# Kernel optimization log

Measured on AMD Instinct MI355X. Metric: run time of the kernel, lower is better.

Reference implementation:

```python
import jax, jax.numpy as jnp
import numpy as np

N_NODES = 20000
N_EDGES = 320000
HIDDEN = 256
N_GRAPHS = 64
IN_DIM = 3
OUT_DIM = 2


def _glorot(key, shape):
    fan_in, fan_out = shape
    lim = jnp.sqrt(6.0 / (fan_in + fan_out))
    return jax.random.uniform(key, shape, jnp.float32, -lim, lim)


def setup_inputs() -> dict:
    key = jax.random.key(0)
    ks = jax.random.split(key, 16)
    inp = {
        "x": jax.random.normal(ks[0], (N_NODES, IN_DIM), jnp.float32),
        "edge_index": jax.random.randint(ks[1], (2, N_EDGES), 0, N_NODES, jnp.int64),
        "batch": jnp.sort(jax.random.randint(ks[2], (N_NODES,), 0, N_GRAPHS, jnp.int64)),
        "W1": _glorot(ks[3], (IN_DIM, HIDDEN)), "b1": jnp.zeros((HIDDEN,), jnp.float32),
        "W2": _glorot(ks[4], (HIDDEN, HIDDEN)), "b2": jnp.zeros((HIDDEN,), jnp.float32),
        "W3": _glorot(ks[5], (HIDDEN, HIDDEN)), "b3": jnp.zeros((HIDDEN,), jnp.float32),
        "W4": _glorot(ks[6], (HIDDEN, HIDDEN)), "b4": jnp.zeros((HIDDEN,), jnp.float32),
        "W5": _glorot(ks[7], (HIDDEN, HIDDEN)), "b5": jnp.zeros((HIDDEN,), jnp.float32),
        "Wlin": _glorot(ks[8], (HIDDEN, OUT_DIM)), "blin": jnp.zeros((OUT_DIM,), jnp.float32),
    }
    return inp


def _gcn_norm(edge_index, n_nodes):
    # PyG GCNConv default: add self-loops, symmetric degree normalization.
    loops = jnp.arange(n_nodes, dtype=edge_index.dtype)
    src = jnp.concatenate([edge_index[0], loops])
    dst = jnp.concatenate([edge_index[1], loops])
    deg = jax.ops.segment_sum(jnp.ones_like(dst, jnp.float32), dst, num_segments=n_nodes)
    dinv = jnp.where(deg > 0, jax.lax.rsqrt(deg), 0.0)
    norm = dinv[src] * dinv[dst]  # [E + N]
    return src, dst, norm


def _gcn_layer(x, W, b, src, dst, norm, n_nodes):
    h = x @ W                                   # [N, H]
    msg = h[src] * norm[:, None]                # [E+N, H] gather + scale
    agg = jax.ops.segment_sum(msg, dst, num_segments=n_nodes)  # scatter-add
    return agg + b


def reference(x, edge_index, batch, W1, b1, W2, b2, W3, b3, W4, b4, W5, b5, Wlin, blin):
    n = x.shape[0]
    src, dst, norm = _gcn_norm(edge_index, n)
    h = jax.nn.relu(_gcn_layer(x, W1, b1, src, dst, norm, n))
    h = jax.nn.relu(_gcn_layer(h, W2, b2, src, dst, norm, n))
    h = jax.nn.relu(_gcn_layer(h, W3, b3, src, dst, norm, n))
    h = jax.nn.relu(_gcn_layer(h, W4, b4, src, dst, norm, n))
    h = jax.nn.relu(_gcn_layer(h, W5, b5, src, dst, norm, n))
    pooled = jax.ops.segment_sum(h, batch, num_segments=N_GRAPHS)  # global_add_pool
    return pooled @ Wlin + blin
```

## Files before the change

kernel.cpp:

```cpp
#include <hip/hip_runtime.h>

#define N_NODES 20000
#define N_PAD 20096
#define N_EDGES 320000
#define HIDDEN 256
#define N_GRAPHS 64
#define OUT_DIM 2

#define QPANEL_BYTES 65536
#define QTABLE_BYTES 32768
#define GEMM_GRID 628

typedef __attribute__((ext_vector_type(8))) short short8v;
typedef __attribute__((ext_vector_type(4))) float f32x4;
typedef __attribute__((ext_vector_type(4))) unsigned short us4;

__global__ void k_zero(int* __restrict__ degi, float* __restrict__ pooled) {
    int i = blockIdx.x * 256 + threadIdx.x;
    if (i < N_NODES) degi[i] = 0;
    if (i < N_GRAPHS * HIDDEN) pooled[i] = 0.f;
}

__global__ void k_degree(const int* __restrict__ dst, int* __restrict__ degi) {
    int e = blockIdx.x * blockDim.x + threadIdx.x;
    if (e < N_EDGES) atomicAdd(&degi[dst[e]], 1);
}

__global__ void k_scan(const int* __restrict__ degi, int* __restrict__ rowptr,
                       int* __restrict__ rowstart, float* __restrict__ dinv) {
    __shared__ int sums[1024];
    int t = threadIdx.x;
    int base = t * 20;
    int ld[20];
    int local = 0;
    if (t < 1000) {
#pragma unroll
        for (int i = 0; i < 20; ++i) {
            ld[i] = degi[base + i];
            local += ld[i];
            dinv[base + i] = rsqrtf((float)ld[i] + 1.0f);
        }
    }
    sums[t] = local;
    __syncthreads();
    for (int off = 1; off < 1024; off <<= 1) {
        int v = (t >= off) ? sums[t - off] : 0;
        __syncthreads();
        sums[t] += v;
        __syncthreads();
    }
    if (t < 1000) {
        int run = (t == 0) ? 0 : sums[t - 1];
#pragma unroll
        for (int i = 0; i < 20; ++i) {
            rowptr[base + i] = run;
            rowstart[base + i] = run;
            run += ld[i];
        }
    }
    if (t == 1023) rowptr[N_NODES] = sums[1023];
}

__global__ void k_fill(const int* __restrict__ src, const int* __restrict__ dst,
                       const float* __restrict__ dinv, int* __restrict__ rowstart,
                       int2* __restrict__ csr) {
    int e = blockIdx.x * blockDim.x + threadIdx.x;
    if (e >= N_EDGES) return;
    int s = src[e], d = dst[e];
    int pos = atomicAdd(&rowstart[d], 1);
    csr[pos] = make_int2(s, __float_as_int(dinv[s] * dinv[d]));
}

__global__ void k_wprep4(const float* __restrict__ W2, const float* __restrict__ W3,
                         const float* __restrict__ W4, const float* __restrict__ W5,
                         char* __restrict__ wt) {
    int lid = blockIdx.x >> 8;
    int idx = (blockIdx.x & 255) * 256 + threadIdx.x;
    const float* W = lid == 0 ? W2 : lid == 1 ? W3 : lid == 2 ? W4 : W5;
    int k = idx & 255, n = idx >> 8;
    float a = W[k * 256 + n];
    unsigned u = __float_as_uint(a);
    ushort hi = (ushort)(u >> 16);
    float hif = __uint_as_float(u & 0xffff0000u);
    ushort lo = (ushort)(__float_as_uint(a - hif) >> 16);
    int q = n >> 6, colQ = n & 63, slab = k >> 3, e = k & 7;
    size_t base = ((size_t)lid * 4 + q) * QPANEL_BYTES;
    size_t soff = (size_t)slab * 1024 + ((colQ * 16 + slab * 32) & 1023) + e * 2;
    *(ushort*)(wt + base + soff) = hi;
    *(ushort*)(wt + base + QTABLE_BYTES + soff) = lo;
}

__global__ void k_aggx(const float* __restrict__ x, const float* __restrict__ dinv,
                       const int* __restrict__ rowptr, const int2* __restrict__ csr,
                       float* __restrict__ z) {
    int t = blockIdx.x * blockDim.x + threadIdx.x;
    int i = t >> 2, c = t & 3;
    if (i >= N_NODES || c >= 3) return;
    float di = dinv[i];
    float a = di * di * x[i * 3 + c], bacc = 0.f;
    int k = rowptr[i], end = rowptr[i + 1];
    for (; k + 1 < end; k += 2) {
        int2 e0 = csr[k], e1 = csr[k + 1];
        a = fmaf(x[(size_t)e0.x * 3 + c], __int_as_float(e0.y), a);
        bacc = fmaf(x[(size_t)e1.x * 3 + c], __int_as_float(e1.y), bacc);
    }
    if (k < end) {
        int2 e0 = csr[k];
        a = fmaf(x[(size_t)e0.x * 3 + c], __int_as_float(e0.y), a);
    }
    z[i * 3 + c] = a + bacc;
}

__global__ void k_h1(const float* __restrict__ z, const float* __restrict__ W1,
                     const float* __restrict__ b1,
                     ushort* __restrict__ out_hi, ushort* __restrict__ out_lo) {
    int i = blockIdx.x;
    int j = threadIdx.x;
    float z0 = z[i * 3], z1 = z[i * 3 + 1], z2 = z[i * 3 + 2];
    float v = fmaf(z0, W1[j], fmaf(z1, W1[256 + j], fmaf(z2, W1[512 + j], b1[j])));
    v = fmaxf(v, 0.0f);
    unsigned u = __float_as_uint(v);
    ushort hi = (ushort)(u >> 16);
    float hif = __uint_as_float(u & 0xffff0000u);
    ushort lo = (ushort)(__float_as_uint(v - hif) >> 16);
    out_hi[(size_t)i * HIDDEN + j] = hi;
    out_lo[(size_t)i * HIDDEN + j] = lo;
}

__global__ void k_csr_agg(const float* __restrict__ h, const float* __restrict__ dinv,
                          const int* __restrict__ rowptr, const int2* __restrict__ csr,
                          const float* __restrict__ b,
                          ushort* __restrict__ out_hi, ushort* __restrict__ out_lo) {
    int bid = blockIdx.x;
    int slice = bid & 7;
    int node = (bid >> 3) * 32 + (threadIdx.x >> 3);
    int cl = threadIdx.x & 7;
    int scol = slice * 32 + cl * 4;
    int beg = rowptr[node], end = rowptr[node + 1];
    float4 A0 = {0.f, 0.f, 0.f, 0.f}, A1 = {0.f, 0.f, 0.f, 0.f};
    int k = beg;
    for (; k + 1 < end; k += 2) {
        int2 e0 = csr[k], e1 = csr[k + 1];
        float w0 = __int_as_float(e0.y), w1 = __int_as_float(e1.y);
        float4 v0 = *reinterpret_cast<const float4*>(h + (size_t)e0.x * HIDDEN + scol);
        float4 v1 = *reinterpret_cast<const float4*>(h + (size_t)e1.x * HIDDEN + scol);
        A0.x = fmaf(v0.x, w0, A0.x);  A1.x = fmaf(v1.x, w1, A1.x);
        A0.y = fmaf(v0.y, w0, A0.y);  A1.y = fmaf(v1.y, w1, A1.y);
        A0.z = fmaf(v0.z, w0, A0.z);  A1.z = fmaf(v1.z, w1, A1.z);
        A0.w = fmaf(v0.w, w0, A0.w);  A1.w = fmaf(v1.w, w1, A1.w);
    }
    if (k < end) {
        int2 e0 = csr[k];
        float w0 = __int_as_float(e0.y);
        float4 v0 = *reinterpret_cast<const float4*>(h + (size_t)e0.x * HIDDEN + scol);
        A0.x = fmaf(v0.x, w0, A0.x);
        A0.y = fmaf(v0.y, w0, A0.y);
        A0.z = fmaf(v0.z, w0, A0.z);
        A0.w = fmaf(v0.w, w0, A0.w);
    }
    float di = dinv[node];
    float ws = di * di;
    float4 bv = *reinterpret_cast<const float4*>(b + scol);
    float4 hv = *reinterpret_cast<const float4*>(h + (size_t)node * HIDDEN + scol);
    float rv[4];
    rv[0] = fmaxf(fmaf(hv.x, ws, bv.x + A0.x + A1.x), 0.f);
    rv[1] = fmaxf(fmaf(hv.y, ws, bv.y + A0.y + A1.y), 0.f);
    rv[2] = fmaxf(fmaf(hv.z, ws, bv.z + A0.z + A1.z), 0.f);
    rv[3] = fmaxf(fmaf(hv.w, ws, bv.w + A0.w + A1.w), 0.f);
    us4 hvv, lvv;
#pragma unroll
    for (int j = 0; j < 4; ++j) {
        unsigned u = __float_as_uint(rv[j]);
        hvv[j] = (ushort)(u >> 16);
        float hif = __uint_as_float(u & 0xffff0000u);
        lvv[j] = (ushort)(__float_as_uint(rv[j] - hif) >> 16);
    }
    *reinterpret_cast<us4*>(out_hi + (size_t)node * HIDDEN + scol) = hvv;
    *reinterpret_cast<us4*>(out_lo + (size_t)node * HIDDEN + scol) = lvv;
}

__global__ __launch_bounds__(512) void k_gemm_mfma(const ushort* __restrict__ a_hi,
                                                   const ushort* __restrict__ a_lo,
                                                   const char* __restrict__ wpanels,
                                                   float* __restrict__ out) {
    __shared__ char smem[QPANEL_BYTES];
    int d = blockIdx.x;
    int xcd = d & 7, idx = d >> 3;
    const int q0 = GEMM_GRID / 8, r = GEMM_GRID % 8;
    int base = xcd * q0 + (xcd < r ? xcd : r);
    int logical = base + idx;
    int mtile = logical >> 2, q = logical & 3;

    const char* gsrc = wpanels + (size_t)q * QPANEL_BYTES;
    int tid = threadIdx.x;
#pragma unroll
    for (int it = 0; it < 8; ++it) {
        int o = it * 8192 + tid * 16;
        *reinterpret_cast<float4*>(smem + o) = *reinterpret_cast<const float4*>(gsrc + o);
    }
    __syncthreads();

    int w = tid >> 6, l = tid & 63;
    int lr = l & 15, kg = l >> 4;
    int wm = w >> 1, wn = w & 1;
    int row0 = mtile * 128 + wm * 32;
    int colQ0 = wn * 32;

    const ushort* aph = a_hi + (size_t)(row0 + lr) * HIDDEN + kg * 8;
    const ushort* apl = a_lo + (size_t)(row0 + lr) * HIDDEN + kg * 8;

    short8v ah0 = *reinterpret_cast<const short8v*>(aph);
    short8v ah1 = *reinterpret_cast<const short8v*>(aph + 16 * HIDDEN);
    short8v al0 = *reinterpret_cast<const short8v*>(apl);
    short8v al1 = *reinterpret_cast<const short8v*>(apl + 16 * HIDDEN);

    f32x4 acc[2][2] = {};
#pragma unroll
    for (int t = 0; t < 8; ++t) {
        short8v cah0 = ah0, cah1 = ah1, cal0 = al0, cal1 = al1;
        if (t < 7) {
            int kb = (t + 1) * 32;
            ah0 = *reinterpret_cast<const short8v*>(aph + kb);
            ah1 = *reinterpret_cast<const short8v*>(aph + 16 * HIDDEN + kb);
            al0 = *reinterpret_cast<const short8v*>(apl + kb);
            al1 = *reinterpret_cast<const short8v*>(apl + 16 * HIDDEN + kb);
        }
        int slab = t * 4 + kg;
        int sbase = slab * 1024;
        int rot = slab * 32;
        int off0 = sbase + (((colQ0 + lr) * 16 + rot) & 1023);
        int off1 = sbase + (((colQ0 + 16 + lr) * 16 + rot) & 1023);
        short8v bh0 = *reinterpret_cast<const short8v*>(smem + off0);
        short8v bh1 = *reinterpret_cast<const short8v*>(smem + off1);
        short8v bl0 = *reinterpret_cast<const short8v*>(smem + QTABLE_BYTES + off0);
        short8v bl1 = *reinterpret_cast<const short8v*>(smem + QTABLE_BYTES + off1);
        acc[0][0] = __builtin_amdgcn_mfma_f32_16x16x32_bf16(cah0, bh0, acc[0][0], 0, 0, 0);
        acc[1][0] = __builtin_amdgcn_mfma_f32_16x16x32_bf16(cah1, bh0, acc[1][0], 0, 0, 0);
        acc[0][1] = __builtin_amdgcn_mfma_f32_16x16x32_bf16(cah0, bh1, acc[0][1], 0, 0, 0);
        acc[1][1] = __builtin_amdgcn_mfma_f32_16x16x32_bf16(cah1, bh1, acc[1][1], 0, 0, 0);
        acc[0][0] = __builtin_amdgcn_mfma_f32_16x16x32_bf16(cal0, bh0, acc[0][0], 0, 0, 0);
        acc[1][0] = __builtin_amdgcn_mfma_f32_16x16x32_bf16(cal1, bh0, acc[1][0], 0, 0, 0);
        acc[0][1] = __builtin_amdgcn_mfma_f32_16x16x32_bf16(cal0, bh1, acc[0][1], 0, 0, 0);
        acc[1][1] = __builtin_amdgcn_mfma_f32_16x16x32_bf16(cal1, bh1, acc[1][1], 0, 0, 0);
        acc[0][0] = __builtin_amdgcn_mfma_f32_16x16x32_bf16(cah0, bl0, acc[0][0], 0, 0, 0);
        acc[1][0] = __builtin_amdgcn_mfma_f32_16x16x32_bf16(cah1, bl0, acc[1][0], 0, 0, 0);
        acc[0][1] = __builtin_amdgcn_mfma_f32_16x16x32_bf16(cah0, bl1, acc[0][1], 0, 0, 0);
        acc[1][1] = __builtin_amdgcn_mfma_f32_16x16x32_bf16(cah1, bl1, acc[1][1], 0, 0, 0);
    }
    int gcol = q * 64 + colQ0 + lr;
#pragma unroll
    for (int rf = 0; rf < 2; ++rf) {
        float* o0 = out + (size_t)(row0 + rf * 16 + kg * 4) * HIDDEN + gcol;
#pragma unroll
        for (int rr = 0; rr < 4; ++rr)
#pragma unroll
            for (int cf = 0; cf < 2; ++cf)
                o0[(size_t)rr * HIDDEN + cf * 16] = acc[rf][cf][rr];
    }
}

__global__ void k_pool(const ushort* __restrict__ hi, const ushort* __restrict__ lo,
                       const int* __restrict__ batch, float* __restrict__ pooled) {
    int base = blockIdx.x * 32;
    int j = threadIdx.x;
    float acc = 0.0f;
    int cur = batch[base];
    for (int r = 0; r < 32; ++r) {
        int i = base + r;
        int bg = batch[i];
        if (bg != cur) {
            atomicAdd(&pooled[cur * HIDDEN + j], acc);
            acc = 0.0f;
            cur = bg;
        }
        size_t off = (size_t)i * HIDDEN + j;
        float v = __uint_as_float((unsigned)hi[off] << 16) +
                  __uint_as_float((unsigned)lo[off] << 16);
        acc += v;
    }
    atomicAdd(&pooled[cur * HIDDEN + j], acc);
}

__global__ void k_final(const float* __restrict__ pooled, const float* __restrict__ Wlin,
                        const float* __restrict__ blin, float* __restrict__ out) {
    int t = threadIdx.x;
    int g = t >> 1, o = t & 1;
    float s = blin[o];
    for (int k = 0; k < HIDDEN; ++k) s += pooled[g * HIDDEN + k] * Wlin[k * OUT_DIM + o];
    out[g * OUT_DIM + o] = s;
}

extern "C" void kernel_launch(void* const* d_in, const int* in_sizes, int n_in,
                              void* d_out, int out_size, void* d_ws, size_t ws_size,
                              hipStream_t stream) {
    const float* x     = (const float*)d_in[0];
    const int*   esrc  = (const int*)d_in[1];
    const int*   edst  = esrc + N_EDGES;
    const int*   batch = (const int*)d_in[2];
    const float* W1 = (const float*)d_in[3];
    const float* b1 = (const float*)d_in[4];
    const float* W2 = (const float*)d_in[5];
    const float* b2 = (const float*)d_in[6];
    const float* W3 = (const float*)d_in[7];
    const float* b3 = (const float*)d_in[8];
    const float* W4 = (const float*)d_in[9];
    const float* b4 = (const float*)d_in[10];
    const float* W5 = (const float*)d_in[11];
    const float* b5 = (const float*)d_in[12];
    const float* Wlin = (const float*)d_in[13];
    const float* blin = (const float*)d_in[14];
    float* out = (float*)d_out;

    char* ws = (char*)d_ws;
    size_t off = 0;
    auto alloc = [&](size_t bytes) { size_t o = off; off += (bytes + 255) & ~size_t(255); return (void*)(ws + o); };

    int*    degi     = (int*)alloc(N_NODES * 4);
    float*  dinv     = (float*)alloc(N_NODES * 4);
    int*    rowptr   = (int*)alloc((N_NODES + 1) * 4);
    int*    rowstart = (int*)alloc(N_NODES * 4);
    int2*   csr      = (int2*)alloc((size_t)N_EDGES * 8);
    float*  hA       = (float*)alloc((size_t)N_PAD * HIDDEN * 4);
    ushort* hb_hi    = (ushort*)alloc((size_t)N_PAD * HIDDEN * 2);
    ushort* hb_lo    = (ushort*)alloc((size_t)N_PAD * HIDDEN * 2);
    float*  pooled   = (float*)alloc(N_GRAPHS * HIDDEN * 4);
    char*   wt       = (char*)alloc((size_t)4 * 4 * QPANEL_BYTES);
    float*  z        = (float*)alloc((size_t)N_NODES * 3 * 4);

    k_zero<<<(N_NODES + 255) / 256, 256, 0, stream>>>(degi, pooled);
    k_degree<<<(N_EDGES + 255) / 256, 256, 0, stream>>>(edst, degi);
    k_scan<<<1, 1024, 0, stream>>>(degi, rowptr, rowstart, dinv);
    k_fill<<<(N_EDGES + 255) / 256, 256, 0, stream>>>(esrc, edst, dinv, rowstart, csr);
    k_wprep4<<<1024, 256, 0, stream>>>(W2, W3, W4, W5, wt);

    const float* bs[5] = {b1, b2, b3, b4, b5};

    k_aggx<<<(N_NODES * 4 + 255) / 256, 256, 0, stream>>>(x, dinv, rowptr, csr, z);
    k_h1<<<N_NODES, HIDDEN, 0, stream>>>(z, W1, b1, hb_hi, hb_lo);

    for (int l = 1; l < 5; ++l) {
        k_gemm_mfma<<<GEMM_GRID, 512, 0, stream>>>(
            hb_hi, hb_lo, wt + (size_t)(l - 1) * 4 * QPANEL_BYTES, hA);
        k_csr_agg<<<(N_NODES / 32) * 8, 256, 0, stream>>>(hA, dinv, rowptr, csr, bs[l], hb_hi, hb_lo);
    }

    k_pool<<<N_NODES / 32, HIDDEN, 0, stream>>>(hb_hi, hb_lo, batch, pooled);
    k_final<<<1, 128, 0, stream>>>(pooled, Wlin, blin, out);
}
```

Measured before the change: 363.3 us.

## Sort nodes by degree for aggregation, unroll gather by four, fuse prep kernels

Builds a degree-bucketed permutation of nodes, using a histogram in the scan kernel and a counting-sort scatter in the fill kernel. Aggregation blocks then process nodes of similar degree together, which cuts wavefront divergence from uneven edge counts. The gather loop is unrolled to four independent accumulators so more loads are in flight. The degree count is merged with weight prep, and the node permutation with the CSR fill, to save launches. The cost is an extra indirection through perm and scattered output writes, since rows are no longer written in node order.

```diff
diff --git a/kernel.cpp b/kernel.cpp
--- a/kernel.cpp
+++ b/kernel.cpp
@@ -21,61 +21,19 @@
     if (i < N_GRAPHS * HIDDEN) pooled[i] = 0.f;
 }
 
-__global__ void k_degree(const int* __restrict__ dst, int* __restrict__ degi) {
-    int e = blockIdx.x * blockDim.x + threadIdx.x;
-    if (e < N_EDGES) atomicAdd(&degi[dst[e]], 1);
-}
-
-__global__ void k_scan(const int* __restrict__ degi, int* __restrict__ rowptr,
-                       int* __restrict__ rowstart, float* __restrict__ dinv) {
-    __shared__ int sums[1024];
-    int t = threadIdx.x;
-    int base = t * 20;
-    int ld[20];
-    int local = 0;
-    if (t < 1000) {
-#pragma unroll
-        for (int i = 0; i < 20; ++i) {
-            ld[i] = degi[base + i];
-            local += ld[i];
-            dinv[base + i] = rsqrtf((float)ld[i] + 1.0f);
-        }
-    }
-    sums[t] = local;
-    __syncthreads();
-    for (int off = 1; off < 1024; off <<= 1) {
-        int v = (t >= off) ? sums[t - off] : 0;
-        __syncthreads();
-        sums[t] += v;
-        __syncthreads();
-    }
-    if (t < 1000) {
-        int run = (t == 0) ? 0 : sums[t - 1];
-#pragma unroll
-        for (int i = 0; i < 20; ++i) {
-            rowptr[base + i] = run;
-            rowstart[base + i] = run;
-            run += ld[i];
-        }
-    }
-    if (t == 1023) rowptr[N_NODES] = sums[1023];
-}
-
-__global__ void k_fill(const int* __restrict__ src, const int* __restrict__ dst,
-                       const float* __restrict__ dinv, int* __restrict__ rowstart,
-                       int2* __restrict__ csr) {
-    int e = blockIdx.x * blockDim.x + threadIdx.x;
-    if (e >= N_EDGES) return;
-    int s = src[e], d = dst[e];
-    int pos = atomicAdd(&rowstart[d], 1);
-    csr[pos] = make_int2(s, __float_as_int(dinv[s] * dinv[d]));
-}
-
-__global__ void k_wprep4(const float* __restrict__ W2, const float* __restrict__ W3,
-                         const float* __restrict__ W4, const float* __restrict__ W5,
-                         char* __restrict__ wt) {
-    int lid = blockIdx.x >> 8;
-    int idx = (blockIdx.x & 255) * 256 + threadIdx.x;
+__global__ void k_degree_wprep(const int* __restrict__ dst, int* __restrict__ degi,
+                               const float* __restrict__ W2, const float* __restrict__ W3,
+                               const float* __restrict__ W4, const float* __restrict__ W5,
+                               char* __restrict__ wt) {
+    int bid = blockIdx.x;
+    if (bid < 1250) {
+        int e = bid * 256 + threadIdx.x;
+        if (e < N_EDGES) atomicAdd(&degi[dst[e]], 1);
+        return;
+    }
+    int wb = bid - 1250;
+    int lid = wb >> 8;
+    int idx = (wb & 255) * 256 + threadIdx.x;
     const float* W = lid == 0 ? W2 : lid == 1 ? W3 : lid == 2 ? W4 : W5;
     int k = idx & 255, n = idx >> 8;
     float a = W[k * 256 + n];
@@ -88,6 +46,72 @@
     size_t soff = (size_t)slab * 1024 + ((colQ * 16 + slab * 32) & 1023) + e * 2;
     *(ushort*)(wt + base + soff) = hi;
     *(ushort*)(wt + base + QTABLE_BYTES + soff) = lo;
+}
+
+__global__ void k_scan(const int* __restrict__ degi, int* __restrict__ rowptr,
+                       int* __restrict__ rowstart, float* __restrict__ dinv,
+                       int* __restrict__ binstart) {
+    __shared__ int sums[1024];
+    __shared__ int bins[256];
+    int t = threadIdx.x;
+    if (t < 256) bins[t] = 0;
+    __syncthreads();
+    int base = t * 20;
+    int ld[20];
+    int local = 0;
+    if (t < 1000) {
+#pragma unroll
+        for (int i = 0; i < 20; ++i) {
+            ld[i] = degi[base + i];
+            local += ld[i];
+            dinv[base + i] = rsqrtf((float)ld[i] + 1.0f);
+            atomicAdd(&bins[ld[i] < 255 ? ld[i] : 255], 1);
+        }
+    }
+    sums[t] = local;
+    __syncthreads();
+    for (int off = 1; off < 1024; off <<= 1) {
+        int v = (t >= off) ? sums[t - off] : 0;
+        __syncthreads();
+        sums[t] += v;
+        __syncthreads();
+    }
+    if (t < 1000) {
+        int run = (t == 0) ? 0 : sums[t - 1];
+#pragma unroll
+        for (int i = 0; i < 20; ++i) {
+            rowptr[base + i] = run;
+            rowstart[base + i] = run;
+            run += ld[i];
+        }
+    }
+    if (t == 1023) rowptr[N_NODES] = sums[1023];
+    __syncthreads();
+    if (t == 0) {
+        int run = 0;
+        for (int i = 0; i < 256; ++i) { binstart[i] = run; run += bins[i]; }
+    }
+}
+
+__global__ void k_fill(const int* __restrict__ src, const int* __restrict__ dst,
+                       const float* __restrict__ dinv, int* __restrict__ rowstart,
+                       int2* __restrict__ csr, const int* __restrict__ degi,
+                       int* __restrict__ binstart, int* __restrict__ perm) {
+    int bid = blockIdx.x;
+    if (bid < 1250) {
+        int e = bid * 256 + threadIdx.x;
+        if (e >= N_EDGES) return;
+        int s = src[e], d = dst[e];
+        int pos = atomicAdd(&rowstart[d], 1);
+        csr[pos] = make_int2(s, __float_as_int(dinv[s] * dinv[d]));
+        return;
+    }
+    int i = (bid - 1250) * 256 + threadIdx.x;
+    if (i < N_NODES) {
+        int d = degi[i]; d = d < 255 ? d : 255;
+        int pos = atomicAdd(&binstart[d], 1);
+        perm[pos] = i;
+    }
 }
 
 __global__ void k_aggx(const float* __restrict__ x, const float* __restrict__ dinv,
@@ -129,17 +153,35 @@
 
 __global__ void k_csr_agg(const float* __restrict__ h, const float* __restrict__ dinv,
                           const int* __restrict__ rowptr, const int2* __restrict__ csr,
-                          const float* __restrict__ b,
+                          const float* __restrict__ b, const int* __restrict__ perm,
                           ushort* __restrict__ out_hi, ushort* __restrict__ out_lo) {
     int bid = blockIdx.x;
     int slice = bid & 7;
-    int node = (bid >> 3) * 32 + (threadIdx.x >> 3);
+    int nidx = (bid >> 3) * 32 + (threadIdx.x >> 3);
+    int node = perm[nidx];
     int cl = threadIdx.x & 7;
     int scol = slice * 32 + cl * 4;
     int beg = rowptr[node], end = rowptr[node + 1];
-    float4 A0 = {0.f, 0.f, 0.f, 0.f}, A1 = {0.f, 0.f, 0.f, 0.f};
+    float4 A0 = {0,0,0,0}, A1 = {0,0,0,0}, A2 = {0,0,0,0}, A3 = {0,0,0,0};
     int k = beg;
-    for (; k + 1 < end; k += 2) {
+    for (; k + 3 < end; k += 4) {
+        int2 e0 = csr[k], e1 = csr[k + 1], e2 = csr[k + 2], e3 = csr[k + 3];
+        float w0 = __int_as_float(e0.y), w1 = __int_as_float(e1.y);
+        float w2 = __int_as_float(e2.y), w3 = __int_as_float(e3.y);
+        float4 v0 = *reinterpret_cast<const float4*>(h + (size_t)e0.x * HIDDEN + scol);
+        float4 v1 = *reinterpret_cast<const float4*>(h + (size_t)e1.x * HIDDEN + scol);
+        float4 v2 = *reinterpret_cast<const float4*>(h + (size_t)e2.x * HIDDEN + scol);
+        float4 v3 = *reinterpret_cast<const float4*>(h + (size_t)e3.x * HIDDEN + scol);
+        A0.x = fmaf(v0.x, w0, A0.x);  A1.x = fmaf(v1.x, w1, A1.x);
+        A0.y = fmaf(v0.y, w0, A0.y);  A1.y = fmaf(v1.y, w1, A1.y);
+        A0.z = fmaf(v0.z, w0, A0.z);  A1.z = fmaf(v1.z, w1, A1.z);
+        A0.w = fmaf(v0.w, w0, A0.w);  A1.w = fmaf(v1.w, w1, A1.w);
+        A2.x = fmaf(v2.x, w2, A2.x);  A3.x = fmaf(v3.x, w3, A3.x);
+        A2.y = fmaf(v2.y, w2, A2.y);  A3.y = fmaf(v3.y, w3, A3.y);
+        A2.z = fmaf(v2.z, w2, A2.z);  A3.z = fmaf(v3.z, w3, A3.z);
+        A2.w = fmaf(v2.w, w2, A2.w);  A3.w = fmaf(v3.w, w3, A3.w);
+    }
+    if (k + 1 < end) {
         int2 e0 = csr[k], e1 = csr[k + 1];
         float w0 = __int_as_float(e0.y), w1 = __int_as_float(e1.y);
         float4 v0 = *reinterpret_cast<const float4*>(h + (size_t)e0.x * HIDDEN + scol);
@@ -148,6 +190,7 @@
         A0.y = fmaf(v0.y, w0, A0.y);  A1.y = fmaf(v1.y, w1, A1.y);
         A0.z = fmaf(v0.z, w0, A0.z);  A1.z = fmaf(v1.z, w1, A1.z);
         A0.w = fmaf(v0.w, w0, A0.w);  A1.w = fmaf(v1.w, w1, A1.w);
+        k += 2;
     }
     if (k < end) {
         int2 e0 = csr[k];
@@ -163,10 +206,10 @@
     float4 bv = *reinterpret_cast<const float4*>(b + scol);
     float4 hv = *reinterpret_cast<const float4*>(h + (size_t)node * HIDDEN + scol);
     float rv[4];
-    rv[0] = fmaxf(fmaf(hv.x, ws, bv.x + A0.x + A1.x), 0.f);
-    rv[1] = fmaxf(fmaf(hv.y, ws, bv.y + A0.y + A1.y), 0.f);
-    rv[2] = fmaxf(fmaf(hv.z, ws, bv.z + A0.z + A1.z), 0.f);
-    rv[3] = fmaxf(fmaf(hv.w, ws, bv.w + A0.w + A1.w), 0.f);
+    rv[0] = fmaxf(fmaf(hv.x, ws, bv.x + (A0.x + A1.x) + (A2.x + A3.x)), 0.f);
+    rv[1] = fmaxf(fmaf(hv.y, ws, bv.y + (A0.y + A1.y) + (A2.y + A3.y)), 0.f);
+    rv[2] = fmaxf(fmaf(hv.z, ws, bv.z + (A0.z + A1.z) + (A2.z + A3.z)), 0.f);
+    rv[3] = fmaxf(fmaf(hv.w, ws, bv.w + (A0.w + A1.w) + (A2.w + A3.w)), 0.f);
     us4 hvv, lvv;
 #pragma unroll
     for (int j = 0; j < 4; ++j) {
@@ -326,12 +369,14 @@
     float*  pooled   = (float*)alloc(N_GRAPHS * HIDDEN * 4);
     char*   wt       = (char*)alloc((size_t)4 * 4 * QPANEL_BYTES);
     float*  z        = (float*)alloc((size_t)N_NODES * 3 * 4);
+    int*    binstart = (int*)alloc(256 * 4);
+    int*    perm     = (int*)alloc(N_NODES * 4);
 
     k_zero<<<(N_NODES + 255) / 256, 256, 0, stream>>>(degi, pooled);
-    k_degree<<<(N_EDGES + 255) / 256, 256, 0, stream>>>(edst, degi);
-    k_scan<<<1, 1024, 0, stream>>>(degi, rowptr, rowstart, dinv);
-    k_fill<<<(N_EDGES + 255) / 256, 256, 0, stream>>>(esrc, edst, dinv, rowstart, csr);
-    k_wprep4<<<1024, 256, 0, stream>>>(W2, W3, W4, W5, wt);
+    k_degree_wprep<<<1250 + 1024, 256, 0, stream>>>(edst, degi, W2, W3, W4, W5, wt);
+    k_scan<<<1, 1024, 0, stream>>>(degi, rowptr, rowstart, dinv, binstart);
+    k_fill<<<1250 + (N_NODES + 255) / 256, 256, 0, stream>>>(
+        esrc, edst, dinv, rowstart, csr, degi, binstart, perm);
 
     const float* bs[5] = {b1, b2, b3, b4, b5};
 
@@ -341,7 +386,8 @@
     for (int l = 1; l < 5; ++l) {
         k_gemm_mfma<<<GEMM_GRID, 512, 0, stream>>>(
             hb_hi, hb_lo, wt + (size_t)(l - 1) * 4 * QPANEL_BYTES, hA);
-        k_csr_agg<<<(N_NODES / 32) * 8, 256, 0, stream>>>(hA, dinv, rowptr, csr, bs[l], hb_hi, hb_lo);
+        k_csr_agg<<<(N_NODES / 32) * 8, 256, 0, stream>>>(
+            hA, dinv, rowptr, csr, bs[l], perm, hb_hi, hb_lo);
     }
 
     k_pool<<<N_NODES / 32, HIDDEN, 0, stream>>>(hb_hi, hb_lo, batch, pooled);
```

Result: slower. 392.5 us (+8.0%).
